# Kernel tuning notes

Measured on AMD Instinct MI355X. Metric: run time of the kernel, lower is better.

Reference implementation:

```python
import jax, jax.numpy as jnp
import numpy as np

NH, HD = 12, 64          # heads, head dim (d_model=768)
SC = HD ** -0.5          # both Attention and CA_Attention use head_dim**-0.5


def patchify(x, p1, p2):
    # 'b c (h p1) (w p2) -> b (h w) (p1 p2 c)'
    B, C, H, W = x.shape
    h, w = H // p1, W // p2
    x = x.reshape(B, C, h, p1, w, p2).transpose(0, 2, 4, 3, 5, 1)  # b h w p1 p2 c
    return x.reshape(B, h * w, p1 * p2 * C)


def unpatchify(x, h, w, p1, p2, c):
    # 'b (h w) (p1 p2 c) -> b c (h p1) (w p2)'
    B = x.shape[0]
    x = x.reshape(B, h, w, p1, p2, c).transpose(0, 5, 1, 3, 2, 4)
    return x.reshape(B, c, h * p1, w * p2)


def ln(x, g, b):
    m = x.mean(-1, keepdims=True)
    v = ((x - m) ** 2).mean(-1, keepdims=True)
    return (x - m) / jnp.sqrt(v + 1e-5) * g + b


def setup_inputs() -> dict:
    key = jax.random.key(0)
    specs = [
        ('img_feats', (2, 32, 112, 112, 80)), ('txt', (2, 77, 768)),
        ('pe_w_ax', (1120, 768)), ('pe_b_ax', (768,)),
        ('pe_w_sag', (1120, 768)), ('pe_b_sag', (768,)),
        ('pe_w_cor', (1568, 768)), ('pe_b_cor', (768,)),
        ('pos_ax', (1, 256, 768)), ('pos_sag', (1, 256, 768)), ('pos_cor', (1, 256, 768)),
        ('qw', (768, 768)), ('kw', (768, 768)), ('vw', (768, 768)),
        ('pw', (768, 768)), ('pb', (768,)),
        ('caq_w', (768, 768)), ('caq_b', (768,)), ('cak_w', (768, 768)), ('cak_b', (768,)),
        ('cav_w', (768, 768)), ('cav_b', (768,)), ('cao_w', (768, 768)), ('cao_b', (768,)),
        ('mlp_w1', (768, 3072)), ('mlp_b1', (3072,)), ('mlp_w2', (3072, 768)), ('mlp_b2', (768,)),
        ('ow_ax', (768, 1120)), ('ob_ax', (1120,)),
        ('ow_sag', (768, 1120)), ('ob_sag', (1120,)),
        ('ow_cor', (768, 1568)), ('ob_cor', (1568,)),
    ]
    big = {'img_feats', 'txt', 'pos_ax', 'pos_sag', 'pos_cor'}
    out = {}
    for k, (n, s) in zip(jax.random.split(key, len(specs)), specs):
        scale = 1.0 if n in big else 0.02
        out[n] = jax.random.normal(k, s, jnp.float32) * scale
    out['view_w'] = jnp.ones((3,), jnp.float32)
    for n in ('n1_g', 'n2_g', 'n3_g'):
        out[n] = jnp.ones((768,), jnp.float32)
    for n in ('n1_b', 'n2_b', 'n3_b'):
        out[n] = jnp.zeros((768,), jnp.float32)
    return out


def reference(img_feats, txt, pe_w_ax, pe_b_ax, pe_w_sag, pe_b_sag, pe_w_cor, pe_b_cor,
              pos_ax, pos_sag, pos_cor, view_w, qw, kw, vw, pw, pb,
              caq_w, caq_b, cak_w, cak_b, cav_w, cav_b, cao_w, cao_b,
              n1_g, n1_b, n2_g, n2_b, n3_g, n3_b,
              mlp_w1, mlp_b1, mlp_w2, mlp_b2,
              ow_ax, ob_ax, ow_sag, ob_sag, ow_cor, ob_cor):

    def img_attn(t):
        B, N, C = t.shape
        q = (t @ qw).reshape(B, N, NH, HD)
        k = (t @ kw).reshape(B, N, NH, HD)
        v = (t @ vw).reshape(B, N, NH, HD)
        a = jax.nn.softmax(jnp.einsum('bnkc,bmkc->bknm', q, k) * SC, axis=-1)
        x = jnp.einsum('bknm,bmkc->bnkc', a, v).reshape(B, N, C)
        return x @ pw + pb

    def ca_attn(t, im):
        B, T, _ = t.shape
        N = im.shape[1]
        qh = (t @ caq_w + caq_b).reshape(B, T, NH, HD).transpose(0, 2, 1, 3)
        kh = (im @ cak_w + cak_b).reshape(B, N, NH, HD).transpose(0, 2, 1, 3)
        vh = (im @ cav_w + cav_b).reshape(B, N, NH, HD).transpose(0, 2, 1, 3)
        a = jax.nn.softmax(jnp.einsum('bhid,bhjd->bhij', qh, kh) * SC, axis=-1)
        # faithful to original einsum 'b h i j, b h j d -> b h j d' (sums over i)
        o = jnp.einsum('bhij,bhjd->bhjd', a, vh)
        o = o.transpose(0, 2, 1, 3).reshape(B, N, NH * HD)
        return o @ cao_w + cao_b

    def branch(v2d, pe_w, pe_b, pos, ow, ob, p1, p2):
        B, C, H, W = v2d.shape
        h, w = H // p1, W // p2
        q = patchify(v2d, p1, p2) @ pe_w + pe_b + pos
        q = ln(q, n1_g, n1_b)
        q = q + img_attn(q)
        q = ln(q, n2_g, n2_b)
        x = q + ca_attn(txt, q)
        x = x + (jax.nn.gelu(ln(x, n3_g, n3_b) @ mlp_w1 + mlp_b1, approximate=False) @ mlp_w2 + mlp_b2)
        return unpatchify(x @ ow + ob, h, w, p1, p2, C)

    # adaptive_avg_pool3d to size-1 along one axis == mean over that axis
    ax = img_feats.mean(2)    # (B,C,H,W)
    sag = img_feats.mean(3)   # (B,C,D,W)
    cor = img_feats.mean(4)   # (B,C,D,H)
    oax = branch(ax, pe_w_ax, pe_b_ax, pos_ax, ow_ax, ob_ax, 7, 5)
    osag = branch(sag, pe_w_sag, pe_b_sag, pos_sag, ow_sag, ob_sag, 7, 5)
    ocor = branch(cor, pe_w_cor, pe_b_cor, pos_cor, ow_cor, ob_cor, 7, 7)
    v3 = (view_w[0] * oax[:, :, None] + view_w[1] * osag[:, :, :, None]
          + view_w[2] * ocor[:, :, :, :, None])
    return img_feats + v3
```

## Files before the change

### kernel.cpp

```cpp
#include <hip/hip_runtime.h>
#include <math.h>

typedef __attribute__((ext_vector_type(8))) short s8;
typedef __attribute__((ext_vector_type(4))) float f4;
typedef unsigned short u16;

__device__ inline u16 f2bf(float f) {
    unsigned u = __float_as_uint(f);
    u += 0x7fffu + ((u >> 16) & 1u);
    return (u16)(u >> 16);
}
__device__ inline float bf2f(u16 x) {
    return __uint_as_float(((unsigned)x) << 16);
}
#define MFMA16(a, b, c) __builtin_amdgcn_mfma_f32_16x16x32_bf16(a, b, c, 0, 0, 0)

__global__ __launch_bounds__(256) void mean3_k(const float* __restrict__ img,
                                               float* __restrict__ axp,
                                               float* __restrict__ sag,
                                               float* __restrict__ cor) {
    __shared__ float sl[112*81];
    int blk = blockIdx.x;
    int dc = blk & 15, bc = blk >> 4;
    int d0 = dc * 7;
    int t = threadIdx.x;
    f4 axr[9];
    #pragma unroll
    for (int k = 0; k < 9; ++k) axr[k] = (f4){0.f,0.f,0.f,0.f};
    const float* base = img + (size_t)bc * 1003520 + (size_t)d0 * 8960;
    for (int sidx = 0; sidx < 7; ++sidx) {
        const f4* sp = reinterpret_cast<const f4*>(base + (size_t)sidx * 8960);
        #pragma unroll
        for (int k = 0; k < 9; ++k) {
            int q = t + k * 256;
            if (q < 2240) {
                f4 v = sp[q];
                axr[k] += v;
                int h = q / 20, w4 = q % 20;
                float* row = &sl[h * 81 + w4 * 4];
                row[0] = v[0]; row[1] = v[1]; row[2] = v[2]; row[3] = v[3];
            }
        }
        __syncthreads();
        if (t < 112) {
            float acc = 0.f;
            #pragma unroll 8
            for (int w = 0; w < 80; ++w) acc += sl[t * 81 + w];
            cor[((size_t)bc * 112 + d0 + sidx) * 112 + t] = acc * (1.f / 80.f);
        } else if (t < 192) {
            int w = t - 112;
            float acc = 0.f;
            #pragma unroll 8
            for (int h = 0; h < 112; ++h) acc += sl[h * 81 + w];
            sag[((size_t)bc * 112 + d0 + sidx) * 80 + w] = acc * (1.f / 112.f);
        }
        __syncthreads();
    }
    float* axo = axp + ((size_t)dc * 64 + bc) * 8960;
    #pragma unroll
    for (int k = 0; k < 9; ++k) {
        int q = t + k * 256;
        if (q < 2240) *reinterpret_cast<f4*>(axo + q * 4) = axr[k];
    }
}

struct TT {
    const float* in[16];
    u16* out[16];
    int K[16];
    int N[16];
    int start[16];
};

__global__ __launch_bounds__(256) void transp_all(TT tab) {
    __shared__ float tl[32][33];
    int bid = blockIdx.x;
    int e = 0;
    #pragma unroll
    for (int i = 1; i < 16; ++i) if (bid >= tab.start[i]) e = i;
    const float* in = tab.in[e];
    u16* out = tab.out[e];
    int K = tab.K[e], N = tab.N[e];
    int tid = bid - tab.start[e];
    int nt = N >> 5;
    int k0 = (tid / nt) * 32, n0 = (tid % nt) * 32;
    int t = threadIdx.x;
    int r = t >> 5, c = t & 31;
    #pragma unroll
    for (int i = 0; i < 4; ++i) tl[r + i*8][c] = in[(long)(k0 + r + i*8)*N + n0 + c];
    __syncthreads();
    #pragma unroll
    for (int i = 0; i < 4; ++i) out[(long)(n0 + r + i*8)*K + k0 + c] = f2bf(tl[c][r + i*8]);
}

__global__ __launch_bounds__(256) void patchify3_k(const float* __restrict__ axp,
                                                   const float* __restrict__ m_sag,
                                                   const float* __restrict__ m_cor,
                                                   u16* __restrict__ P0, u16* __restrict__ P1,
                                                   u16* __restrict__ P2) {
    __shared__ float sl[32][113];
    int br = blockIdx.y;
    int X = blockIdx.x;
    int b = X / 112, rem = X % 112;
    int hh = rem / 7, pp1 = rem % 7;
    const float* src; u16* dst; int Wt, p2, PD;
    if (br == 0)      { src = nullptr; dst = P0; Wt = 80;  p2 = 5; PD = 1120; }
    else if (br == 1) { src = m_sag;   dst = P1; Wt = 80;  p2 = 5; PD = 1120; }
    else              { src = m_cor;   dst = P2; Wt = 112; p2 = 7; PD = 1568; }
    int t = threadIdx.x;
    int row = hh*7 + pp1;
    int wq = Wt >> 2;
    if (br == 0) {
        for (int i = t; i < 32*20; i += 256) {
            int c = i / 20, w4 = i % 20;
            f4 s = (f4){0.f,0.f,0.f,0.f};
            size_t base = ((size_t)(b*32 + c)*112 + row)*80 + w4*4;
            #pragma unroll
            for (int p = 0; p < 16; ++p)
                s += *reinterpret_cast<const f4*>(axp + (size_t)p*573440 + base);
            s *= (1.f/112.f);
            sl[c][w4*4+0] = s[0]; sl[c][w4*4+1] = s[1]; sl[c][w4*4+2] = s[2]; sl[c][w4*4+3] = s[3];
        }
    } else {
        for (int i = t; i < 32*wq; i += 256) {
            int c = i / wq, w4 = i % wq;
            float4 v = *reinterpret_cast<const float4*>(
                src + ((size_t)(b*32 + c)*112 + row)*Wt + w4*4);
            sl[c][w4*4+0] = v.x; sl[c][w4*4+1] = v.y; sl[c][w4*4+2] = v.z; sl[c][w4*4+3] = v.w;
        }
    }
    __syncthreads();
    int tot = 16 * p2 * 32;
    for (int o = t; o < tot; o += 256) {
        int ww = o / (p2*32), rest = o % (p2*32);
        int pp2 = rest >> 5, c = rest & 31;
        dst[((size_t)(b*256 + hh*16 + ww))*PD + (pp1*p2 + pp2)*32 + c]
            = f2bf(sl[c][ww*p2 + pp2]);
    }
}

__device__ inline void load_tile(const u16* __restrict__ P, int ld, int nrows, int K,
                                 int r0, int k0, int t, s8 v[4]) {
    #pragma unroll
    for (int i = 0; i < 4; ++i) {
        int chunk = t + i*256;
        int row = chunk >> 4, c8 = (chunk & 15) * 8;
        s8 x;
        #pragma unroll
        for (int q = 0; q < 8; ++q) x[q] = 0;
        if (r0 + row < nrows && k0 + c8 < K)
            x = *reinterpret_cast<const s8*>(P + (long)(r0 + row)*ld + k0 + c8);
        v[i] = x;
    }
}
__device__ inline void load_tile_f32(const float* __restrict__ P, int ld, int nrows, int K,
                                     int r0, int k0, int t, s8 v[4]) {
    #pragma unroll
    for (int i = 0; i < 4; ++i) {
        int chunk = t + i*256;
        int row = chunk >> 4, c8 = (chunk & 15) * 8;
        s8 x;
        #pragma unroll
        for (int q = 0; q < 8; ++q) x[q] = 0;
        if (r0 + row < nrows && k0 + c8 < K) {
            const float* src = P + (long)(r0 + row)*ld + k0 + c8;
            #pragma unroll
            for (int q = 0; q < 8; ++q) x[q] = (short)f2bf(src[q]);
        }
        v[i] = x;
    }
}
__device__ inline void write_tile(u16 (*S)[136], int t, const s8 v[4]) {
    #pragma unroll
    for (int i = 0; i < 4; ++i) {
        int chunk = t + i*256;
        *reinterpret_cast<s8*>(&S[chunk >> 4][(chunk & 15)*8]) = v[i];
    }
}
__device__ inline void mfma_tile(const u16 (*As)[136], const u16 (*Bs)[136],
                                 int wr, int wc, int lane, f4 acc[2][2]) {
    int lrow = lane & 15;
    #pragma unroll
    for (int kh = 0; kh < 4; ++kh) {
        int lk = kh*32 + (lane >> 4) * 8;
        s8 af0 = *reinterpret_cast<const s8*>(&As[wr*32 + lrow][lk]);
        s8 af1 = *reinterpret_cast<const s8*>(&As[wr*32 + 16 + lrow][lk]);
        s8 bg0 = *reinterpret_cast<const s8*>(&Bs[wc*32 + lrow][lk]);
        s8 bg1 = *reinterpret_cast<const s8*>(&Bs[wc*32 + 16 + lrow][lk]);
        acc[0][0] = MFMA16(af0, bg0, acc[0][0]);
        acc[0][1] = MFMA16(af0, bg1, acc[0][1]);
        acc[1][0] = MFMA16(af1, bg0, acc[1][0]);
        acc[1][1] = MFMA16(af1, bg1, acc[1][1]);
    }
}

__global__ __launch_bounds__(256) void gemm_bf(
    const u16* __restrict__ A, const u16* __restrict__ Bt,
    float* __restrict__ Cf, u16* __restrict__ Cb,
    int M, int N, int K,
    const float* __restrict__ bias, const float* __restrict__ resid,
    int act)
{
    __shared__ u16 As[2][64][136];
    __shared__ u16 Bs[2][64][136];
    int t = threadIdx.x;
    int m0 = blockIdx.y * 64, n0 = blockIdx.x * 64;
    int wave = t >> 6, lane = t & 63;
    int wr = wave >> 1, wc = wave & 1;
    f4 acc[2][2];
    #pragma unroll
    for (int m = 0; m < 2; ++m)
        #pragma unroll
        for (int n = 0; n < 2; ++n)
            #pragma unroll
            for (int r = 0; r < 4; ++r) acc[m][n][r] = 0.f;
    int nk = (K + 127) >> 7;
    s8 pa[4], pbv[4];
    load_tile(A, K, M, K, m0, 0, t, pa);
    load_tile(Bt, K, N, K, n0, 0, t, pbv);
    write_tile(As[0], t, pa);
    write_tile(Bs[0], t, pbv);
    __syncthreads();
    for (int kt = 0; kt < nk; ++kt) {
        int cur = kt & 1;
        if (kt + 1 < nk) {
            load_tile(A, K, M, K, m0, (kt+1) << 7, t, pa);
            load_tile(Bt, K, N, K, n0, (kt+1) << 7, t, pbv);
        }
        mfma_tile(As[cur], Bs[cur], wr, wc, lane, acc);
        if (kt + 1 < nk) {
            write_tile(As[cur^1], t, pa);
            write_tile(Bs[cur^1], t, pbv);
        }
        __syncthreads();
    }
    #pragma unroll
    for (int m = 0; m < 2; ++m) {
        int rbase = m0 + wr*32 + m*16 + (lane >> 4) * 4;
        #pragma unroll
        for (int n = 0; n < 2; ++n) {
            int col = n0 + wc*32 + n*16 + (lane & 15);
            if (col >= N) continue;
            #pragma unroll
            for (int r = 0; r < 4; ++r) {
                int row = rbase + r;
                if (row >= M) continue;
                float v = acc[m][n][r];
                if (bias)  v += bias[col];
                if (resid) v += resid[(long)row * N + col];
                if (act == 1) v = 0.5f * v * (1.0f + erff(v * 0.70710678118654752f));
                long ci = (long)row * N + col;
                if (Cf) Cf[ci] = v;
                if (Cb) Cb[ci] = f2bf(v);
            }
        }
    }
}

__global__ __launch_bounds__(256) void gemm_big(
    const u16* __restrict__ A, const u16* __restrict__ Bt,
    u16* __restrict__ Cb, u16* __restrict__ vt,
    int N, int K,
    const float* __restrict__ bias, const float* __restrict__ bias2, int act)
{
    __shared__ u16 As[2][128][72];
    __shared__ u16 Bs[2][128][72];
    int t = threadIdx.x;
    int m0 = blockIdx.y * 128, n0 = blockIdx.x * 128;
    int wave = t >> 6, lane = t & 63;
    int wr = wave >> 1, wc = wave & 1;
    f4 acc[4][4];
    #pragma unroll
    for (int m = 0; m < 4; ++m)
        #pragma unroll
        for (int n = 0; n < 4; ++n)
            #pragma unroll
            for (int r = 0; r < 4; ++r) acc[m][n][r] = 0.f;
    int nk = K >> 6;
    s8 pa[4], pbv[4];
    #pragma unroll
    for (int i = 0; i < 4; ++i) {
        int chunk = t + i*256;
        pa[i]  = *reinterpret_cast<const s8*>(A  + (long)(m0 + (chunk>>3))*K + (chunk&7)*8);
        pbv[i] = *reinterpret_cast<const s8*>(Bt + (long)(n0 + (chunk>>3))*K + (chunk&7)*8);
    }
    #pragma unroll
    for (int i = 0; i < 4; ++i) {
        int chunk = t + i*256;
        *reinterpret_cast<s8*>(&As[0][chunk>>3][(chunk&7)*8]) = pa[i];
        *reinterpret_cast<s8*>(&Bs[0][chunk>>3][(chunk&7)*8]) = pbv[i];
    }
    __syncthreads();
    for (int kt = 0; kt < nk; ++kt) {
        int cur = kt & 1;
        if (kt + 1 < nk) {
            int k0 = (kt+1) << 6;
            #pragma unroll
            for (int i = 0; i < 4; ++i) {
                int chunk = t + i*256;
                pa[i]  = *reinterpret_cast<const s8*>(A  + (long)(m0 + (chunk>>3))*K + k0 + (chunk&7)*8);
                pbv[i] = *reinterpret_cast<const s8*>(Bt + (long)(n0 + (chunk>>3))*K + k0 + (chunk&7)*8);
            }
        }
        #pragma unroll
        for (int kh = 0; kh < 2; ++kh) {
            int lk = kh*32 + (lane >> 4) * 8;
            int lr = lane & 15;
            s8 af[4], bf[4];
            #pragma unroll
            for (int m = 0; m < 4; ++m)
                af[m] = *reinterpret_cast<const s8*>(&As[cur][wr*64 + m*16 + lr][lk]);
            #pragma unroll
            for (int n = 0; n < 4; ++n)
                bf[n] = *reinterpret_cast<const s8*>(&Bs[cur][wc*64 + n*16 + lr][lk]);
            #pragma unroll
            for (int m = 0; m < 4; ++m)
                #pragma unroll
                for (int n = 0; n < 4; ++n)
                    acc[m][n] = MFMA16(af[m], bf[n], acc[m][n]);
        }
        if (kt + 1 < nk) {
            #pragma unroll
            for (int i = 0; i < 4; ++i) {
                int chunk = t + i*256;
                *reinterpret_cast<s8*>(&As[cur^1][chunk>>3][(chunk&7)*8]) = pa[i];
                *reinterpret_cast<s8*>(&Bs[cur^1][chunk>>3][(chunk&7)*8]) = pbv[i];
            }
        }
        __syncthreads();
    }
    #pragma unroll
    for (int m = 0; m < 4; ++m) {
        int rbase = m0 + wr*64 + m*16 + (lane >> 4) * 4;
        #pragma unroll
        for (int n = 0; n < 4; ++n) {
            int col = n0 + wc*64 + n*16 + (lane & 15);
            #pragma unroll
            for (int r = 0; r < 4; ++r) {
                int row = rbase + r;
                float v = acc[m][n][r];
                if (bias) {
                    float bb = bias2 ? ((col < 768) ? bias[col] : bias2[col - 768]) : bias[col];
                    v += bb;
                }
                if (act == 1) v = 0.5f * v * (1.0f + erff(v * 0.70710678118654752f));
                u16 b = f2bf(v);
                Cb[(long)row * N + col] = b;
                if (vt && col >= 1536) {
                    int z = (row >> 8) * 12 + ((col - 1536) >> 6);
                    vt[((long)z * 64 + (col & 63)) * 256 + (row & 255)] = b;
                }
            }
        }
    }
}

struct PeDesc {
    const u16* A[3];
    const u16* Bt[4];
    const float* bias[4];
    const float* pos[3];
    int K[4];
    int M[4];
};

__global__ __launch_bounds__(256) void gemm_pe(PeDesc d, const float* __restrict__ txtf,
                                               float* __restrict__ C, u16* __restrict__ QHb) {
    int z = blockIdx.z;
    int M = d.M[z], K = d.K[z];
    int m0 = blockIdx.y * 64, n0 = blockIdx.x * 64;
    if (m0 >= M) return;
    __shared__ u16 As[2][64][136];
    __shared__ u16 Bs[2][64][136];
    const u16* Bb = d.Bt[z];
    const float* bias = d.bias[z];
    int t = threadIdx.x;
    int wave = t >> 6, lane = t & 63;
    int wr = wave >> 1, wc = wave & 1;
    f4 acc[2][2];
    #pragma unroll
    for (int m = 0; m < 2; ++m)
        #pragma unroll
        for (int n = 0; n < 2; ++n)
            #pragma unroll
            for (int r = 0; r < 4; ++r) acc[m][n][r] = 0.f;
    int nk = (K + 127) >> 7;
    s8 pa[4], pbv[4];
    if (z < 3) load_tile(d.A[z], K, M, K, m0, 0, t, pa);
    else       load_tile_f32(txtf, K, M, K, m0, 0, t, pa);
    load_tile(Bb, K, 768, K, n0, 0, t, pbv);
    write_tile(As[0], t, pa);
    write_tile(Bs[0], t, pbv);
    __syncthreads();
    for (int kt = 0; kt < nk; ++kt) {
        int cur = kt & 1;
        if (kt + 1 < nk) {
            if (z < 3) load_tile(d.A[z], K, M, K, m0, (kt+1) << 7, t, pa);
            else       load_tile_f32(txtf, K, M, K, m0, (kt+1) << 7, t, pa);
            load_tile(Bb, K, 768, K, n0, (kt+1) << 7, t, pbv);
        }
        mfma_tile(As[cur], Bs[cur], wr, wc, lane, acc);
        if (kt + 1 < nk) {
            write_tile(As[cur^1], t, pa);
            write_tile(Bs[cur^1], t, pbv);
        }
        __syncthreads();
    }
    #pragma unroll
    for (int m = 0; m < 2; ++m) {
        int rbase = m0 + wr*32 + m*16 + (lane >> 4) * 4;
        #pragma unroll
        for (int n = 0; n < 2; ++n) {
            int col = n0 + wc*32 + n*16 + (lane & 15);
            #pragma unroll
            for (int r = 0; r < 4; ++r) {
                int row = rbase + r;
                if (row >= M) continue;
                float v = acc[m][n][r] + bias[col];
                if (z < 3) {
                    v += d.pos[z][(long)(row & 255)*768 + col];
                    C[((long)z*512 + row) * 768 + col] = v;
                } else {
                    QHb[(long)row * 768 + col] = f2bf(v);
                }
            }
        }
    }
}

struct OwDesc {
    const u16* Bt[3];
    float* plane[3];
    const float* bias[3];
    int N[3];
    int p2[3];
    int Wd[3];
};

__global__ __launch_bounds__(256) void gemm_ow(OwDesc d, const u16* __restrict__ A,
                                               const float* __restrict__ vwp) {
    int z = blockIdx.z;
    int N = d.N[z];
    int n0 = blockIdx.x * 64;
    if (n0 >= N) return;
    __shared__ u16 As[2][64][136];
    __shared__ u16 Bs[2][64][136];
    const u16* Ab = A + (long)z * 512 * 768;
    const u16* Bb = d.Bt[z];
    int t = threadIdx.x;
    int m0 = blockIdx.y * 64;
    int wave = t >> 6, lane = t & 63;
    int wr = wave >> 1, wc = wave & 1;
    f4 acc[2][2];
    #pragma unroll
    for (int m = 0; m < 2; ++m)
        #pragma unroll
        for (int n = 0; n < 2; ++n)
            #pragma unroll
            for (int r = 0; r < 4; ++r) acc[m][n][r] = 0.f;
    s8 pa[4], pbv[4];
    load_tile(Ab, 768, 512, 768, m0, 0, t, pa);
    load_tile(Bb, 768, N, 768, n0, 0, t, pbv);
    write_tile(As[0], t, pa);
    write_tile(Bs[0], t, pbv);
    __syncthreads();
    for (int kt = 0; kt < 6; ++kt) {
        int cur = kt & 1;
        if (kt + 1 < 6) {
            load_tile(Ab, 768, 512, 768, m0, (kt+1) << 7, t, pa);
            load_tile(Bb, 768, N, 768, n0, (kt+1) << 7, t, pbv);
        }
        mfma_tile(As[cur], Bs[cur], wr, wc, lane, acc);
        if (kt + 1 < 6) {
            write_tile(As[cur^1], t, pa);
            write_tile(Bs[cur^1], t, pbv);
        }
        __syncthreads();
    }
    float* plane = d.plane[z];
    const float* bias = d.bias[z];
    int p2 = d.p2[z], Wd = d.Wd[z];
    float wt = vwp[z];
    #pragma unroll
    for (int m = 0; m < 2; ++m) {
        int rbase = m0 + wr*32 + m*16 + (lane >> 4) * 4;
        #pragma unroll
        for (int n = 0; n < 2; ++n) {
            int col = n0 + wc*32 + n*16 + (lane & 15);
            if (col >= N) continue;
            int pp = col >> 5, c = col & 31;
            int pp1 = pp / p2, pp2 = pp % p2;
            float bv = bias[col];
            #pragma unroll
            for (int r = 0; r < 4; ++r) {
                int row = rbase + r;
                int b = row >> 8, nn = row & 255;
                int hh = nn >> 4, ww = nn & 15;
                int ho = hh*7 + pp1, wo = ww*p2 + pp2;
                plane[((long)(b*32 + c)*112 + ho)*Wd + wo] = wt * (acc[m][n][r] + bv);
            }
        }
    }
}

__global__ __launch_bounds__(256) void ln_k(const float* __restrict__ in,
                                            float* __restrict__ outf,
                                            u16* __restrict__ outb,
                                            const float* __restrict__ g,
                                            const float* __restrict__ bta) {
    constexpr int N = 768;
    int row = blockIdx.x;
    const float* x = in + (size_t)row * N;
    int t = threadIdx.x;
    float v0 = x[t], v1 = x[t+256], v2 = x[t+512];
    float s = v0+v1+v2, s2 = v0*v0+v1*v1+v2*v2;
    #pragma unroll
    for (int off = 32; off > 0; off >>= 1) { s += __shfl_down(s, off); s2 += __shfl_down(s2, off); }
    __shared__ float red[8];
    int wid = t >> 6, lane = t & 63;
    if (lane == 0) { red[wid] = s; red[wid+4] = s2; }
    __syncthreads();
    if (t == 0) {
        float S = red[0]+red[1]+red[2]+red[3];
        float S2 = red[4]+red[5]+red[6]+red[7];
        float mean = S * (1.f/N);
        float var = S2 * (1.f/N) - mean*mean;
        red[0] = mean; red[1] = rsqrtf(var + 1e-5f);
    }
    __syncthreads();
    float mean = red[0], rstd = red[1];
    float y0 = (v0-mean)*rstd*g[t]     + bta[t];
    float y1 = (v1-mean)*rstd*g[t+256] + bta[t+256];
    float y2 = (v2-mean)*rstd*g[t+512] + bta[t+512];
    if (outf) {
        float* y = outf + (size_t)row * N;
        y[t] = y0; y[t+256] = y1; y[t+512] = y2;
    }
    if (outb) {
        u16* y = outb + (size_t)row * N;
        y[t] = f2bf(y0); y[t+256] = f2bf(y1); y[t+512] = f2bf(y2);
    }
}

__global__ __launch_bounds__(256) void attn_k(const u16* __restrict__ QKV,
                                              const u16* __restrict__ Vt,
                                              u16* __restrict__ O) {
    __shared__ u16 Ks[256][72];
    __shared__ u16 Ps[128][264];
    __shared__ u16 Vs[64][264];
    int zz = blockIdx.x;
    int bh = zz >> 1, half = zz & 1;
    int bb = bh / 12, h = bh % 12;
    long qrow0 = (long)bb*256 + half*128;
    int hcol = h*64;
    int t = threadIdx.x;
    int wave = t >> 6, lane = t & 63;
    int lr = lane & 15, lg = lane >> 4;
    #pragma unroll
    for (int i = 0; i < 8; ++i) {
        int chunk = t + i*256;
        int row = chunk >> 3, c8 = (chunk & 7)*8;
        *reinterpret_cast<s8*>(&Ks[row][c8]) =
            *reinterpret_cast<const s8*>(QKV + ((long)bb*256 + row)*2304 + 768 + hcol + c8);
    }
    #pragma unroll
    for (int i = 0; i < 8; ++i) {
        int chunk = t + i*256;
        int d = chunk >> 5, j8 = (chunk & 31)*8;
        *reinterpret_cast<s8*>(&Vs[d][j8]) =
            *reinterpret_cast<const s8*>(Vt + (long)bh*16384 + (long)d*256 + j8);
    }
    __syncthreads();
    f4 acc[2][16];
    #pragma unroll
    for (int m = 0; m < 2; ++m)
        #pragma unroll
        for (int n = 0; n < 16; ++n)
            #pragma unroll
            for (int r = 0; r < 4; ++r) acc[m][n][r] = 0.f;
    #pragma unroll
    for (int kh = 0; kh < 2; ++kh) {
        s8 af0 = *reinterpret_cast<const s8*>(QKV + (qrow0 + wave*32 + lr)*2304 + hcol + kh*32 + lg*8);
        s8 af1 = *reinterpret_cast<const s8*>(QKV + (qrow0 + wave*32 + 16 + lr)*2304 + hcol + kh*32 + lg*8);
        #pragma unroll
        for (int n = 0; n < 16; ++n) {
            s8 bf = *reinterpret_cast<const s8*>(&Ks[n*16 + lr][kh*32 + lg*8]);
            acc[0][n] = MFMA16(af0, bf, acc[0][n]);
            acc[1][n] = MFMA16(af1, bf, acc[1][n]);
        }
    }
    #pragma unroll
    for (int m = 0; m < 2; ++m)
        #pragma unroll
        for (int r = 0; r < 4; ++r) {
            float mx = -1e30f;
            #pragma unroll
            for (int n = 0; n < 16; ++n) mx = fmaxf(mx, acc[m][n][r]);
            #pragma unroll
            for (int o = 8; o; o >>= 1) mx = fmaxf(mx, __shfl_xor(mx, o));
            float l = 0.f;
            float p[16];
            #pragma unroll
            for (int n = 0; n < 16; ++n) {
                p[n] = __expf((acc[m][n][r] - mx) * 0.125f);
                l += p[n];
            }
            #pragma unroll
            for (int o = 8; o; o >>= 1) l += __shfl_xor(l, o);
            float inv = 1.f / l;
            int prow = wave*32 + m*16 + lg*4 + r;
            #pragma unroll
            for (int n = 0; n < 16; ++n)
                Ps[prow][n*16 + lr] = f2bf(p[n] * inv);
        }
    __syncthreads();
    f4 o2[2][4];
    #pragma unroll
    for (int m = 0; m < 2; ++m)
        #pragma unroll
        for (int n = 0; n < 4; ++n)
            #pragma unroll
            for (int r = 0; r < 4; ++r) o2[m][n][r] = 0.f;
    #pragma unroll
    for (int kh = 0; kh < 8; ++kh) {
        s8 pf0 = *reinterpret_cast<const s8*>(&Ps[wave*32 + lr][kh*32 + lg*8]);
        s8 pf1 = *reinterpret_cast<const s8*>(&Ps[wave*32 + 16 + lr][kh*32 + lg*8]);
        #pragma unroll
        for (int n = 0; n < 4; ++n) {
            s8 vf = *reinterpret_cast<const s8*>(&Vs[n*16 + lr][kh*32 + lg*8]);
            o2[0][n] = MFMA16(pf0, vf, o2[0][n]);
            o2[1][n] = MFMA16(pf1, vf, o2[1][n]);
        }
    }
    #pragma unroll
    for (int m = 0; m < 2; ++m)
        #pragma unroll
        for (int n = 0; n < 4; ++n)
            #pragma unroll
            for (int r = 0; r < 4; ++r)
                O[(qrow0 + wave*32 + m*16 + lg*4 + r)*768 + hcol + n*16 + lr] = f2bf(o2[m][n][r]);
}

__global__ __launch_bounds__(256) void ca_fused(const u16* __restrict__ QHb,
                                                const u16* __restrict__ KVHb,
                                                u16* __restrict__ O) {
    __shared__ u16 QHs[80][72];
    __shared__ u16 KHs[256][72];
    __shared__ float rmax[80][4];
    __shared__ float rsum[80][4];
    __shared__ float Wj[256];
    int bh = blockIdx.x;
    int rowblk = bh / 12, h = bh % 12;
    int bsel = rowblk & 1;
    int t = threadIdx.x;
    int wave = t >> 6, lane = t & 63;
    int lr = lane & 15, lg = lane >> 4;
    #pragma unroll
    for (int i = 0; i < 3; ++i) {
        int chunk = t + i*256;
        if (chunk < 640) {
            int row = chunk >> 3, c8 = (chunk & 7)*8;
            s8 v;
            #pragma unroll
            for (int q = 0; q < 8; ++q) v[q] = 0;
            if (row < 77)
                v = *reinterpret_cast<const s8*>(QHb + ((long)(bsel*77 + row))*768 + h*64 + c8);
            *reinterpret_cast<s8*>(&QHs[row][c8]) = v;
        }
    }
    #pragma unroll
    for (int i = 0; i < 8; ++i) {
        int chunk = t + i*256;
        int row = chunk >> 3, c8 = (chunk & 7)*8;
        *reinterpret_cast<s8*>(&KHs[row][c8]) =
            *reinterpret_cast<const s8*>(KVHb + ((long)rowblk*256 + row)*1536 + h*64 + c8);
    }
    __syncthreads();
    f4 acc[5][4];
    #pragma unroll
    for (int m = 0; m < 5; ++m)
        #pragma unroll
        for (int n = 0; n < 4; ++n)
            #pragma unroll
            for (int r = 0; r < 4; ++r) acc[m][n][r] = 0.f;
    #pragma unroll
    for (int kh = 0; kh < 2; ++kh) {
        s8 af[5], bf[4];
        #pragma unroll
        for (int m = 0; m < 5; ++m)
            af[m] = *reinterpret_cast<const s8*>(&QHs[m*16 + lr][kh*32 + lg*8]);
        #pragma unroll
        for (int n = 0; n < 4; ++n)
            bf[n] = *reinterpret_cast<const s8*>(&KHs[wave*64 + n*16 + lr][kh*32 + lg*8]);
        #pragma unroll
        for (int m = 0; m < 5; ++m)
            #pragma unroll
            for (int n = 0; n < 4; ++n)
                acc[m][n] = MFMA16(af[m], bf[n], acc[m][n]);
    }
    #pragma unroll
    for (int m = 0; m < 5; ++m)
        #pragma unroll
        for (int r = 0; r < 4; ++r) {
            float mx = -1e30f;
            #pragma unroll
            for (int n = 0; n < 4; ++n) mx = fmaxf(mx, acc[m][n][r]);
            #pragma unroll
            for (int o = 8; o; o >>= 1) mx = fmaxf(mx, __shfl_xor(mx, o));
            if (lr == 0) rmax[m*16 + lg*4 + r][wave] = mx;
        }
    __syncthreads();
    #pragma unroll
    for (int m = 0; m < 5; ++m)
        #pragma unroll
        for (int r = 0; r < 4; ++r) {
            int i = m*16 + lg*4 + r;
            float mi = fmaxf(fmaxf(rmax[i][0], rmax[i][1]), fmaxf(rmax[i][2], rmax[i][3]));
            float s = 0.f;
            #pragma unroll
            for (int n = 0; n < 4; ++n) s += __expf((acc[m][n][r] - mi) * 0.125f);
            #pragma unroll
            for (int o = 8; o; o >>= 1) s += __shfl_xor(s, o);
            if (lr == 0) rsum[i][wave] = s;
        }
    __syncthreads();
    float wn[4] = {0.f, 0.f, 0.f, 0.f};
    #pragma unroll
    for (int m = 0; m < 5; ++m)
        #pragma unroll
        for (int r = 0; r < 4; ++r) {
            int i = m*16 + lg*4 + r;
            if (i < 77) {
                float mi = fmaxf(fmaxf(rmax[i][0], rmax[i][1]), fmaxf(rmax[i][2], rmax[i][3]));
                float li = rsum[i][0] + rsum[i][1] + rsum[i][2] + rsum[i][3];
                float inv = 1.f / li;
                #pragma unroll
                for (int n = 0; n < 4; ++n)
                    wn[n] += __expf((acc[m][n][r] - mi) * 0.125f) * inv;
            }
        }
    #pragma unroll
    for (int n = 0; n < 4; ++n) {
        wn[n] += __shfl_xor(wn[n], 16);
        wn[n] += __shfl_xor(wn[n], 32);
    }
    if (lane < 16) {
        #pragma unroll
        for (int n = 0; n < 4; ++n) Wj[wave*64 + n*16 + lr] = wn[n];
    }
    __syncthreads();
    int d = t & 63;
    #pragma unroll 4
    for (int it = 0; it < 64; ++it) {
        int j = it*4 + (t >> 6);
        long row = (long)rowblk*256 + j;
        float vh = bf2f(KVHb[row*1536 + 768 + h*64 + d]);
        O[row*768 + h*64 + d] = f2bf(Wj[j] * vh);
    }
}

__global__ __launch_bounds__(256) void final_k(const float* __restrict__ img,
                                               const float* __restrict__ Aax,
                                               const float* __restrict__ Asag,
                                               const float* __restrict__ Acor,
                                               float* __restrict__ out) {
    int blk = blockIdx.x;
    int bc = blk / 112;
    const float4* ip = reinterpret_cast<const float4*>(img + (size_t)blk * 8960);
    const float4* ap = reinterpret_cast<const float4*>(Aax + (size_t)bc * 8960);
    const float4* sp = reinterpret_cast<const float4*>(Asag + (size_t)blk * 80);
    const float*  cp = Acor + (size_t)blk * 112;
    float4* op = reinterpret_cast<float4*>(out + (size_t)blk * 8960);
    int t = threadIdx.x;
    for (int q = t; q < 2240; q += 256) {
        int h = q / 20, w4 = q % 20;
        float4 iv = ip[q], av = ap[q], sv = sp[w4];
        float cv = cp[h];
        float4 o;
        o.x = iv.x + av.x + sv.x + cv;
        o.y = iv.y + av.y + sv.y + cv;
        o.z = iv.z + av.z + sv.z + cv;
        o.w = iv.w + av.w + sv.w + cv;
        op[q] = o;
    }
}

extern "C" void kernel_launch(void* const* d_in, const int* in_sizes, int n_in,
                              void* d_out, int out_size, void* d_ws, size_t ws_size,
                              hipStream_t stream) {
    (void)in_sizes; (void)n_in; (void)out_size; (void)ws_size;
    const float* img    = (const float*)d_in[0];
    const float* txt    = (const float*)d_in[1];
    const float* pe_w[3] = {(const float*)d_in[2], (const float*)d_in[4], (const float*)d_in[6]};
    const float* pe_b[3] = {(const float*)d_in[3], (const float*)d_in[5], (const float*)d_in[7]};
    const float* pos[3]  = {(const float*)d_in[8], (const float*)d_in[9], (const float*)d_in[10]};
    const float* qw = (const float*)d_in[11];
    const float* kw = (const float*)d_in[12];
    const float* vw_attn = (const float*)d_in[13];
    const float* pw = (const float*)d_in[14];
    const float* pb = (const float*)d_in[15];
    const float* caq_w = (const float*)d_in[16];
    const float* caq_b = (const float*)d_in[17];
    const float* cak_w = (const float*)d_in[18];
    const float* cak_b = (const float*)d_in[19];
    const float* cav_w = (const float*)d_in[20];
    const float* cav_b = (const float*)d_in[21];
    const float* cao_w = (const float*)d_in[22];
    const float* cao_b = (const float*)d_in[23];
    const float* mlp_w1 = (const float*)d_in[24];
    const float* mlp_b1 = (const float*)d_in[25];
    const float* mlp_w2 = (const float*)d_in[26];
    const float* mlp_b2 = (const float*)d_in[27];
    const float* ow[3] = {(const float*)d_in[28], (const float*)d_in[30], (const float*)d_in[32]};
    const float* ob[3] = {(const float*)d_in[29], (const float*)d_in[31], (const float*)d_in[33]};
    const float* view_w = (const float*)d_in[34];
    const float* n_g[3] = {(const float*)d_in[35], (const float*)d_in[36], (const float*)d_in[37]};
    const float* n_b[3] = {(const float*)d_in[38], (const float*)d_in[39], (const float*)d_in[40]};

    unsigned char* sb = (unsigned char*)d_out;
    size_t off = 0;
    auto B = [&](size_t bytes) -> void* {
        void* p = sb + off; off += (bytes + 511) & ~(size_t)511; return p;
    };
    u16* qkvT  = (u16*)B((size_t)2304*768*2);
    u16* pwT   = (u16*)B(768*768*2);
    u16* caqT  = (u16*)B(768*768*2);
    u16* cakvT = (u16*)B((size_t)1536*768*2);
    u16* caoT  = (u16*)B(768*768*2);
    u16* mlp1T = (u16*)B((size_t)3072*768*2);
    u16* mlp2T = (u16*)B((size_t)768*3072*2);
    u16* peT[3]; peT[0] = (u16*)B((size_t)768*1120*2); peT[1] = (u16*)B((size_t)768*1120*2); peT[2] = (u16*)B((size_t)768*1568*2);
    u16* owT[3]; owT[0] = (u16*)B((size_t)1120*768*2); owT[1] = (u16*)B((size_t)1120*768*2); owT[2] = (u16*)B((size_t)1568*768*2);
    float* axp   = (float*)B((size_t)16*573440*4);
    float* m_sag = (float*)B(573440*4);
    float* m_cor = (float*)B(802816*4);
    u16* P0 = (u16*)B((size_t)512*1120*2);
    u16* P1 = (u16*)B((size_t)512*1120*2);
    u16* P2 = (u16*)B((size_t)512*1568*2);
    float* X0  = (float*)B((size_t)1536*768*4);
    float* X1f = (float*)B((size_t)1536*768*4);
    float* X2  = (float*)B((size_t)1536*768*4);
    float* X3f = (float*)B((size_t)1536*768*4);
    float* X4  = (float*)B((size_t)1536*768*4);
    u16* X1b = (u16*)B((size_t)1536*768*2);
    u16* X3b = (u16*)B((size_t)1536*768*2);
    u16* X5b = (u16*)B((size_t)1536*768*2);
    u16* X6b = (u16*)B((size_t)1536*768*2);
    u16* QKVb = (u16*)B((size_t)1536*2304*2);
    u16* Obf = (u16*)B((size_t)1536*768*2);
    u16* Vt  = (u16*)B((size_t)72*64*256*2);
    u16* Hb  = (u16*)B((size_t)1536*3072*2);
    u16* KVHb = (u16*)B((size_t)1536*1536*2);
    u16* QHb  = (u16*)B((size_t)154*768*2);

    float* ws = (float*)d_ws;
    float* Aax  = ws;
    float* Asag = ws + 573440;
    float* Acor = ws + 1146880;

    TT tab;
    {
        const float* ins[16] = {qw, kw, vw_attn, pw, caq_w, cak_w, cav_w, cao_w,
                                mlp_w1, mlp_w2, pe_w[0], pe_w[1], pe_w[2], ow[0], ow[1], ow[2]};
        u16* outs[16] = {qkvT, qkvT + 768*768, qkvT + 2*768*768, pwT, caqT, cakvT,
                         cakvT + 768*768, caoT, mlp1T, mlp2T, peT[0], peT[1], peT[2],
                         owT[0], owT[1], owT[2]};
        int Ks[16] = {768,768,768,768,768,768,768,768, 768,3072, 1120,1120,1568, 768,768,768};
        int Ns[16] = {768,768,768,768,768,768,768,768, 3072,768, 768,768,768, 1120,1120,1568};
        int st = 0;
        for (int i = 0; i < 16; ++i) {
            tab.in[i] = ins[i]; tab.out[i] = outs[i]; tab.K[i] = Ks[i]; tab.N[i] = Ns[i];
            tab.start[i] = st;
            st += (Ks[i] >> 5) * (Ns[i] >> 5);
        }
        transp_all<<<st, 256, 0, stream>>>(tab);
    }

    mean3_k<<<1024, 256, 0, stream>>>(img, axp, m_sag, m_cor);
    patchify3_k<<<dim3(224,3), 256, 0, stream>>>(axp, m_sag, m_cor, P0, P1, P2);

    auto gemm = [&](const u16* A, const u16* Bt, float* Cf, u16* Cb,
                    int M, int N, int K, const float* bias, const float* resid, int act) {
        dim3 g((N+63)/64, (M+63)/64, 1);
        gemm_bf<<<g, 256, 0, stream>>>(A, Bt, Cf, Cb, M, N, K, bias, resid, act);
    };

    {
        PeDesc d;
        d.A[0] = P0; d.A[1] = P1; d.A[2] = P2;
        d.Bt[0] = peT[0]; d.Bt[1] = peT[1]; d.Bt[2] = peT[2]; d.Bt[3] = caqT;
        d.bias[0] = pe_b[0]; d.bias[1] = pe_b[1]; d.bias[2] = pe_b[2]; d.bias[3] = caq_b;
        d.pos[0] = pos[0]; d.pos[1] = pos[1]; d.pos[2] = pos[2];
        d.K[0] = 1120; d.K[1] = 1120; d.K[2] = 1568; d.K[3] = 768;
        d.M[0] = 512; d.M[1] = 512; d.M[2] = 512; d.M[3] = 154;
        gemm_pe<<<dim3(12,8,4), 256, 0, stream>>>(d, txt, X0, QHb);
    }

    ln_k<<<1536, 256, 0, stream>>>(X0, X1f, X1b, n_g[0], n_b[0]);
    gemm_big<<<dim3(18,12), 256, 0, stream>>>(X1b, qkvT, QKVb, Vt, 2304, 768, nullptr, nullptr, 0);
    attn_k<<<144, 256, 0, stream>>>(QKVb, Vt, Obf);
    gemm(Obf, pwT, X2, nullptr, 1536, 768, 768, pb, X1f, 0);
    ln_k<<<1536, 256, 0, stream>>>(X2, X3f, X3b, n_g[1], n_b[1]);
    gemm_big<<<dim3(12,12), 256, 0, stream>>>(X3b, cakvT, KVHb, nullptr, 1536, 768, cak_b, cav_b, 0);
    ca_fused<<<72, 256, 0, stream>>>(QHb, KVHb, Obf);
    gemm(Obf, caoT, X4, nullptr, 1536, 768, 768, cao_b, X3f, 0);
    ln_k<<<1536, 256, 0, stream>>>(X4, nullptr, X5b, n_g[2], n_b[2]);
    gemm_big<<<dim3(24,12), 256, 0, stream>>>(X5b, mlp1T, Hb, nullptr, 3072, 768, mlp_b1, nullptr, 1);
    gemm(Hb, mlp2T, nullptr, X6b, 1536, 768, 3072, mlp_b2, X4, 0);
    {
        OwDesc d;
        d.Bt[0] = owT[0]; d.Bt[1] = owT[1]; d.Bt[2] = owT[2];
        d.plane[0] = Aax; d.plane[1] = Asag; d.plane[2] = Acor;
        d.bias[0] = ob[0]; d.bias[1] = ob[1]; d.bias[2] = ob[2];
        d.N[0] = 1120; d.N[1] = 1120; d.N[2] = 1568;
        d.p2[0] = 5; d.p2[1] = 5; d.p2[2] = 7;
        d.Wd[0] = 80; d.Wd[1] = 80; d.Wd[2] = 112;
        gemm_ow<<<dim3(25,8,3), 256, 0, stream>>>(d, X6b, view_w);
    }

    final_k<<<7168, 256, 0, stream>>>(img, Aax, Asag, Acor, (float*)d_out);
}
```

Measured before the change: 445.9 us.

## Merge mean and weight-transpose kernels; route big GEMMs through 64x64 gemm_bf

Folds the weight-transpose kernel and the 3-axis mean kernel into one launch, with block index ranges picking the work, so the two run concurrently and one launch is saved. Removes the 128x128 gemm_big kernel and sends the QKV, CA K/V and MLP1 GEMMs through the generic 64x64-tile gemm_bf, which gains bias2 and V-transpose epilogue support. The smaller tiles give more blocks for these mid-size GEMMs, at the cost of less register reuse per block and a heavier shared-memory footprint in the fused prep kernel.

```diff
diff --git a/kernel.cpp b/kernel.cpp
--- a/kernel.cpp
+++ b/kernel.cpp
@@ -14,55 +14,6 @@
     return __uint_as_float(((unsigned)x) << 16);
 }
 #define MFMA16(a, b, c) __builtin_amdgcn_mfma_f32_16x16x32_bf16(a, b, c, 0, 0, 0)
-
-__global__ __launch_bounds__(256) void mean3_k(const float* __restrict__ img,
-                                               float* __restrict__ axp,
-                                               float* __restrict__ sag,
-                                               float* __restrict__ cor) {
-    __shared__ float sl[112*81];
-    int blk = blockIdx.x;
-    int dc = blk & 15, bc = blk >> 4;
-    int d0 = dc * 7;
-    int t = threadIdx.x;
-    f4 axr[9];
-    #pragma unroll
-    for (int k = 0; k < 9; ++k) axr[k] = (f4){0.f,0.f,0.f,0.f};
-    const float* base = img + (size_t)bc * 1003520 + (size_t)d0 * 8960;
-    for (int sidx = 0; sidx < 7; ++sidx) {
-        const f4* sp = reinterpret_cast<const f4*>(base + (size_t)sidx * 8960);
-        #pragma unroll
-        for (int k = 0; k < 9; ++k) {
-            int q = t + k * 256;
-            if (q < 2240) {
-                f4 v = sp[q];
-                axr[k] += v;
-                int h = q / 20, w4 = q % 20;
-                float* row = &sl[h * 81 + w4 * 4];
-                row[0] = v[0]; row[1] = v[1]; row[2] = v[2]; row[3] = v[3];
-            }
-        }
-        __syncthreads();
-        if (t < 112) {
-            float acc = 0.f;
-            #pragma unroll 8
-            for (int w = 0; w < 80; ++w) acc += sl[t * 81 + w];
-            cor[((size_t)bc * 112 + d0 + sidx) * 112 + t] = acc * (1.f / 80.f);
-        } else if (t < 192) {
-            int w = t - 112;
-            float acc = 0.f;
-            #pragma unroll 8
-            for (int h = 0; h < 112; ++h) acc += sl[h * 81 + w];
-            sag[((size_t)bc * 112 + d0 + sidx) * 80 + w] = acc * (1.f / 112.f);
-        }
-        __syncthreads();
-    }
-    float* axo = axp + ((size_t)dc * 64 + bc) * 8960;
-    #pragma unroll
-    for (int k = 0; k < 9; ++k) {
-        int q = t + k * 256;
-        if (q < 2240) *reinterpret_cast<f4*>(axo + q * 4) = axr[k];
-    }
-}
 
 struct TT {
     const float* in[16];
@@ -70,21 +21,70 @@
     int K[16];
     int N[16];
     int start[16];
+    int total;
 };
 
-__global__ __launch_bounds__(256) void transp_all(TT tab) {
-    __shared__ float tl[32][33];
+__global__ __launch_bounds__(256) void prep_k(TT tab, const float* __restrict__ img,
+                                              float* __restrict__ axp,
+                                              float* __restrict__ sag,
+                                              float* __restrict__ cor) {
+    __shared__ float sl[112*81];
     int bid = blockIdx.x;
+    int t = threadIdx.x;
+    if (bid < 1024) {
+        int dc = bid & 15, bc = bid >> 4;
+        int d0 = dc * 7;
+        f4 axr[9];
+        #pragma unroll
+        for (int k = 0; k < 9; ++k) axr[k] = (f4){0.f,0.f,0.f,0.f};
+        const float* base = img + (size_t)bc * 1003520 + (size_t)d0 * 8960;
+        for (int sidx = 0; sidx < 7; ++sidx) {
+            const f4* sp = reinterpret_cast<const f4*>(base + (size_t)sidx * 8960);
+            #pragma unroll
+            for (int k = 0; k < 9; ++k) {
+                int q = t + k * 256;
+                if (q < 2240) {
+                    f4 v = sp[q];
+                    axr[k] += v;
+                    int h = q / 20, w4 = q % 20;
+                    float* row = &sl[h * 81 + w4 * 4];
+                    row[0] = v[0]; row[1] = v[1]; row[2] = v[2]; row[3] = v[3];
+                }
+            }
+            __syncthreads();
+            if (t < 112) {
+                float acc = 0.f;
+                #pragma unroll 8
+                for (int w = 0; w < 80; ++w) acc += sl[t * 81 + w];
+                cor[((size_t)bc * 112 + d0 + sidx) * 112 + t] = acc * (1.f / 80.f);
+            } else if (t < 192) {
+                int w = t - 112;
+                float acc = 0.f;
+                #pragma unroll 8
+                for (int h = 0; h < 112; ++h) acc += sl[h * 81 + w];
+                sag[((size_t)bc * 112 + d0 + sidx) * 80 + w] = acc * (1.f / 112.f);
+            }
+            __syncthreads();
+        }
+        float* axo = axp + ((size_t)dc * 64 + bc) * 8960;
+        #pragma unroll
+        for (int k = 0; k < 9; ++k) {
+            int q = t + k * 256;
+            if (q < 2240) *reinterpret_cast<f4*>(axo + q * 4) = axr[k];
+        }
+        return;
+    }
+    int tb = bid - 1024;
+    float (*tl)[33] = reinterpret_cast<float(*)[33]>(sl);
     int e = 0;
     #pragma unroll
-    for (int i = 1; i < 16; ++i) if (bid >= tab.start[i]) e = i;
+    for (int i = 1; i < 16; ++i) if (tb >= tab.start[i]) e = i;
     const float* in = tab.in[e];
     u16* out = tab.out[e];
     int K = tab.K[e], N = tab.N[e];
-    int tid = bid - tab.start[e];
+    int tid = tb - tab.start[e];
     int nt = N >> 5;
     int k0 = (tid / nt) * 32, n0 = (tid % nt) * 32;
-    int t = threadIdx.x;
     int r = t >> 5, c = t & 31;
     #pragma unroll
     for (int i = 0; i < 4; ++i) tl[r + i*8][c] = in[(long)(k0 + r + i*8)*N + n0 + c];
@@ -198,8 +198,8 @@
     const u16* __restrict__ A, const u16* __restrict__ Bt,
     float* __restrict__ Cf, u16* __restrict__ Cb,
     int M, int N, int K,
-    const float* __restrict__ bias, const float* __restrict__ resid,
-    int act)
+    const float* __restrict__ bias, const float* __restrict__ bias2,
+    const float* __restrict__ resid, int act, u16* __restrict__ vt)
 {
     __shared__ u16 As[2][64][136];
     __shared__ u16 Bs[2][64][136];
@@ -246,106 +246,16 @@
                 int row = rbase + r;
                 if (row >= M) continue;
                 float v = acc[m][n][r];
-                if (bias)  v += bias[col];
-                if (resid) v += resid[(long)row * N + col];
-                if (act == 1) v = 0.5f * v * (1.0f + erff(v * 0.70710678118654752f));
-                long ci = (long)row * N + col;
-                if (Cf) Cf[ci] = v;
-                if (Cb) Cb[ci] = f2bf(v);
-            }
-        }
-    }
-}
-
-__global__ __launch_bounds__(256) void gemm_big(
-    const u16* __restrict__ A, const u16* __restrict__ Bt,
-    u16* __restrict__ Cb, u16* __restrict__ vt,
-    int N, int K,
-    const float* __restrict__ bias, const float* __restrict__ bias2, int act)
-{
-    __shared__ u16 As[2][128][72];
-    __shared__ u16 Bs[2][128][72];
-    int t = threadIdx.x;
-    int m0 = blockIdx.y * 128, n0 = blockIdx.x * 128;
-    int wave = t >> 6, lane = t & 63;
-    int wr = wave >> 1, wc = wave & 1;
-    f4 acc[4][4];
-    #pragma unroll
-    for (int m = 0; m < 4; ++m)
-        #pragma unroll
-        for (int n = 0; n < 4; ++n)
-            #pragma unroll
-            for (int r = 0; r < 4; ++r) acc[m][n][r] = 0.f;
-    int nk = K >> 6;
-    s8 pa[4], pbv[4];
-    #pragma unroll
-    for (int i = 0; i < 4; ++i) {
-        int chunk = t + i*256;
-        pa[i]  = *reinterpret_cast<const s8*>(A  + (long)(m0 + (chunk>>3))*K + (chunk&7)*8);
-        pbv[i] = *reinterpret_cast<const s8*>(Bt + (long)(n0 + (chunk>>3))*K + (chunk&7)*8);
-    }
-    #pragma unroll
-    for (int i = 0; i < 4; ++i) {
-        int chunk = t + i*256;
-        *reinterpret_cast<s8*>(&As[0][chunk>>3][(chunk&7)*8]) = pa[i];
-        *reinterpret_cast<s8*>(&Bs[0][chunk>>3][(chunk&7)*8]) = pbv[i];
-    }
-    __syncthreads();
-    for (int kt = 0; kt < nk; ++kt) {
-        int cur = kt & 1;
-        if (kt + 1 < nk) {
-            int k0 = (kt+1) << 6;
-            #pragma unroll
-            for (int i = 0; i < 4; ++i) {
-                int chunk = t + i*256;
-                pa[i]  = *reinterpret_cast<const s8*>(A  + (long)(m0 + (chunk>>3))*K + k0 + (chunk&7)*8);
-                pbv[i] = *reinterpret_cast<const s8*>(Bt + (long)(n0 + (chunk>>3))*K + k0 + (chunk&7)*8);
-            }
-        }
-        #pragma unroll
-        for (int kh = 0; kh < 2; ++kh) {
-            int lk = kh*32 + (lane >> 4) * 8;
-            int lr = lane & 15;
-            s8 af[4], bf[4];
-            #pragma unroll
-            for (int m = 0; m < 4; ++m)
-                af[m] = *reinterpret_cast<const s8*>(&As[cur][wr*64 + m*16 + lr][lk]);
-            #pragma unroll
-            for (int n = 0; n < 4; ++n)
-                bf[n] = *reinterpret_cast<const s8*>(&Bs[cur][wc*64 + n*16 + lr][lk]);
-            #pragma unroll
-            for (int m = 0; m < 4; ++m)
-                #pragma unroll
-                for (int n = 0; n < 4; ++n)
-                    acc[m][n] = MFMA16(af[m], bf[n], acc[m][n]);
-        }
-        if (kt + 1 < nk) {
-            #pragma unroll
-            for (int i = 0; i < 4; ++i) {
-                int chunk = t + i*256;
-                *reinterpret_cast<s8*>(&As[cur^1][chunk>>3][(chunk&7)*8]) = pa[i];
-                *reinterpret_cast<s8*>(&Bs[cur^1][chunk>>3][(chunk&7)*8]) = pbv[i];
-            }
-        }
-        __syncthreads();
-    }
-    #pragma unroll
-    for (int m = 0; m < 4; ++m) {
-        int rbase = m0 + wr*64 + m*16 + (lane >> 4) * 4;
-        #pragma unroll
-        for (int n = 0; n < 4; ++n) {
-            int col = n0 + wc*64 + n*16 + (lane & 15);
-            #pragma unroll
-            for (int r = 0; r < 4; ++r) {
-                int row = rbase + r;
-                float v = acc[m][n][r];
                 if (bias) {
                     float bb = bias2 ? ((col < 768) ? bias[col] : bias2[col - 768]) : bias[col];
                     v += bb;
                 }
+                if (resid) v += resid[(long)row * N + col];
                 if (act == 1) v = 0.5f * v * (1.0f + erff(v * 0.70710678118654752f));
+                long ci = (long)row * N + col;
                 u16 b = f2bf(v);
-                Cb[(long)row * N + col] = b;
+                if (Cf) Cf[ci] = v;
+                if (Cb) Cb[ci] = b;
                 if (vt && col >= 1536) {
                     int z = (row >> 8) * 12 + ((col - 1536) >> 6);
                     vt[((long)z * 64 + (col & 63)) * 256 + (row & 255)] = b;
@@ -496,8 +406,8 @@
                 int row = rbase + r;
                 int b = row >> 8, nn = row & 255;
                 int hh = nn >> 4, ww = nn & 15;
-                int ho = hh*7 + pp1, wo = ww*p2 + pp2;
-                plane[((long)(b*32 + c)*112 + ho)*Wd + wo] = wt * (acc[m][n][r] + bv);
+                plane[((long)(b*32 + c)*112 + hh*7 + pp1)*Wd + ww*p2 + pp2]
+                    = wt * (acc[m][n][r] + bv);
             }
         }
     }
@@ -817,41 +727,42 @@
     const float* n_g[3] = {(const float*)d_in[35], (const float*)d_in[36], (const float*)d_in[37]};
     const float* n_b[3] = {(const float*)d_in[38], (const float*)d_in[39], (const float*)d_in[40]};
 
+    typedef unsigned short u16t;
     unsigned char* sb = (unsigned char*)d_out;
     size_t off = 0;
     auto B = [&](size_t bytes) -> void* {
         void* p = sb + off; off += (bytes + 511) & ~(size_t)511; return p;
     };
-    u16* qkvT  = (u16*)B((size_t)2304*768*2);
-    u16* pwT   = (u16*)B(768*768*2);
-    u16* caqT  = (u16*)B(768*768*2);
-    u16* cakvT = (u16*)B((size_t)1536*768*2);
-    u16* caoT  = (u16*)B(768*768*2);
-    u16* mlp1T = (u16*)B((size_t)3072*768*2);
-    u16* mlp2T = (u16*)B((size_t)768*3072*2);
-    u16* peT[3]; peT[0] = (u16*)B((size_t)768*1120*2); peT[1] = (u16*)B((size_t)768*1120*2); peT[2] = (u16*)B((size_t)768*1568*2);
-    u16* owT[3]; owT[0] = (u16*)B((size_t)1120*768*2); owT[1] = (u16*)B((size_t)1120*768*2); owT[2] = (u16*)B((size_t)1568*768*2);
+    u16t* qkvT  = (u16t*)B((size_t)2304*768*2);
+    u16t* pwT   = (u16t*)B(768*768*2);
+    u16t* caqT  = (u16t*)B(768*768*2);
+    u16t* cakvT = (u16t*)B((size_t)1536*768*2);
+    u16t* caoT  = (u16t*)B(768*768*2);
+    u16t* mlp1T = (u16t*)B((size_t)3072*768*2);
+    u16t* mlp2T = (u16t*)B((size_t)768*3072*2);
+    u16t* peT[3]; peT[0] = (u16t*)B((size_t)768*1120*2); peT[1] = (u16t*)B((size_t)768*1120*2); peT[2] = (u16t*)B((size_t)768*1568*2);
+    u16t* owT[3]; owT[0] = (u16t*)B((size_t)1120*768*2); owT[1] = (u16t*)B((size_t)1120*768*2); owT[2] = (u16t*)B((size_t)1568*768*2);
     float* axp   = (float*)B((size_t)16*573440*4);
     float* m_sag = (float*)B(573440*4);
     float* m_cor = (float*)B(802816*4);
-    u16* P0 = (u16*)B((size_t)512*1120*2);
-    u16* P1 = (u16*)B((size_t)512*1120*2);
-    u16* P2 = (u16*)B((size_t)512*1568*2);
+    u16t* P0 = (u16t*)B((size_t)512*1120*2);
+    u16t* P1 = (u16t*)B((size_t)512*1120*2);
+    u16t* P2 = (u16t*)B((size_t)512*1568*2);
     float* X0  = (float*)B((size_t)1536*768*4);
     float* X1f = (float*)B((size_t)1536*768*4);
     float* X2  = (float*)B((size_t)1536*768*4);
     float* X3f = (float*)B((size_t)1536*768*4);
     float* X4  = (float*)B((size_t)1536*768*4);
-    u16* X1b = (u16*)B((size_t)1536*768*2);
-    u16* X3b = (u16*)B((size_t)1536*768*2);
-    u16* X5b = (u16*)B((size_t)1536*768*2);
-    u16* X6b = (u16*)B((size_t)1536*768*2);
-    u16* QKVb = (u16*)B((size_t)1536*2304*2);
-    u16* Obf = (u16*)B((size_t)1536*768*2);
-    u16* Vt  = (u16*)B((size_t)72*64*256*2);
-    u16* Hb  = (u16*)B((size_t)1536*3072*2);
-    u16* KVHb = (u16*)B((size_t)1536*1536*2);
-    u16* QHb  = (u16*)B((size_t)154*768*2);
+    u16t* X1b = (u16t*)B((size_t)1536*768*2);
+    u16t* X3b = (u16t*)B((size_t)1536*768*2);
+    u16t* X5b = (u16t*)B((size_t)1536*768*2);
+    u16t* X6b = (u16t*)B((size_t)1536*768*2);
+    u16t* QKVb = (u16t*)B((size_t)1536*2304*2);
+    u16t* Obf = (u16t*)B((size_t)1536*768*2);
+    u16t* Vt  = (u16t*)B((size_t)72*64*256*2);
+    u16t* Hb  = (u16t*)B((size_t)1536*3072*2);
+    u16t* KVHb = (u16t*)B((size_t)1536*1536*2);
+    u16t* QHb  = (u16t*)B((size_t)154*768*2);
 
     float* ws = (float*)d_ws;
     float* Aax  = ws;
@@ -862,9 +773,9 @@
     {
         const float* ins[16] = {qw, kw, vw_attn, pw, caq_w, cak_w, cav_w, cao_w,
                                 mlp_w1, mlp_w2, pe_w[0], pe_w[1], pe_w[2], ow[0], ow[1], ow[2]};
-        u16* outs[16] = {qkvT, qkvT + 768*768, qkvT + 2*768*768, pwT, caqT, cakvT,
-                         cakvT + 768*768, caoT, mlp1T, mlp2T, peT[0], peT[1], peT[2],
-                         owT[0], owT[1], owT[2]};
+        u16t* outs[16] = {qkvT, qkvT + 768*768, qkvT + 2*768*768, pwT, caqT, cakvT,
+                          cakvT + 768*768, caoT, mlp1T, mlp2T, peT[0], peT[1], peT[2],
+                          owT[0], owT[1], owT[2]};
         int Ks[16] = {768,768,768,768,768,768,768,768, 768,3072, 1120,1120,1568, 768,768,768};
         int Ns[16] = {768,768,768,768,768,768,768,768, 3072,768, 768,768,768, 1120,1120,1568};
         int st = 0;
@@ -873,16 +784,17 @@
             tab.start[i] = st;
             st += (Ks[i] >> 5) * (Ns[i] >> 5);
         }
-        transp_all<<<st, 256, 0, stream>>>(tab);
-    }
-
-    mean3_k<<<1024, 256, 0, stream>>>(img, axp, m_sag, m_cor);
+        tab.total = st;
+        prep_k<<<1024 + st, 256, 0, stream>>>(tab, img, axp, m_sag, m_cor);
+    }
+
     patchify3_k<<<dim3(224,3), 256, 0, stream>>>(axp, m_sag, m_cor, P0, P1, P2);
 
-    auto gemm = [&](const u16* A, const u16* Bt, float* Cf, u16* Cb,
-                    int M, int N, int K, const float* bias, const float* resid, int act) {
+    auto gemm = [&](const u16t* A, const u16t* Bt, float* Cf, u16t* Cb,
+                    int M, int N, int K, const float* bias, const float* bias2,
+                    const float* resid, int act, u16t* vt) {
         dim3 g((N+63)/64, (M+63)/64, 1);
-        gemm_bf<<<g, 256, 0, stream>>>(A, Bt, Cf, Cb, M, N, K, bias, resid, act);
+        gemm_bf<<<g, 256, 0, stream>>>(A, Bt, Cf, Cb, M, N, K, bias, bias2, resid, act, vt);
     };
 
     {
@@ -897,16 +809,16 @@
     }
 
     ln_k<<<1536, 256, 0, stream>>>(X0, X1f, X1b, n_g[0], n_b[0]);
-    gemm_big<<<dim3(18,12), 256, 0, stream>>>(X1b, qkvT, QKVb, Vt, 2304, 768, nullptr, nullptr, 0);
+    gemm(X1b, qkvT, nullptr, QKVb, 1536, 2304, 768, nullptr, nullptr, nullptr, 0, Vt);
     attn_k<<<144, 256, 0, stream>>>(QKVb, Vt, Obf);
-    gemm(Obf, pwT, X2, nullptr, 1536, 768, 768, pb, X1f, 0);
+    gemm(Obf, pwT, X2, nullptr, 1536, 768, 768, pb, nullptr, X1f, 0, nullptr);
     ln_k<<<1536, 256, 0, stream>>>(X2, X3f, X3b, n_g[1], n_b[1]);
-    gemm_big<<<dim3(12,12), 256, 0, stream>>>(X3b, cakvT, KVHb, nullptr, 1536, 768, cak_b, cav_b, 0);
+    gemm(X3b, cakvT, nullptr, KVHb, 1536, 1536, 768, cak_b, cav_b, nullptr, 0, nullptr);
     ca_fused<<<72, 256, 0, stream>>>(QHb, KVHb, Obf);
-    gemm(Obf, caoT, X4, nullptr, 1536, 768, 768, cao_b, X3f, 0);
+    gemm(Obf, caoT, X4, nullptr, 1536, 768, 768, cao_b, nullptr, X3f, 0, nullptr);
     ln_k<<<1536, 256, 0, stream>>>(X4, nullptr, X5b, n_g[2], n_b[2]);
-    gemm_big<<<dim3(24,12), 256, 0, stream>>>(X5b, mlp1T, Hb, nullptr, 3072, 768, mlp_b1, nullptr, 1);
-    gemm(Hb, mlp2T, nullptr, X6b, 1536, 768, 3072, mlp_b2, X4, 0);
+    gemm(X5b, mlp1T, nullptr, Hb, 1536, 3072, 768, mlp_b1, nullptr, nullptr, 1, nullptr);
+    gemm(Hb, mlp2T, nullptr, X6b, 1536, 768, 3072, mlp_b2, nullptr, X4, 0, nullptr);
     {
         OwDesc d;
         d.Bt[0] = owT[0]; d.Bt[1] = owT[1]; d.Bt[2] = owT[2];
```

Measured after the change: 439.8 us. No clear change (-1.4%).
